# Performance work log

Hardware: AMD Instinct MI355X
Metric: run time of the kernel (lower is better)

Reference implementation:

```python
import jax, jax.numpy as jnp
import numpy as np

N_NODES = 50000
N_EDGES = 800000
D_IN = 256
DIM_H = 256
N_GRAPHS = 500
N_OUT = 10
BN_EPS = 1e-5


def _mlp(h, W1, b1, gamma, beta, mean, var, W2, b2):
    # Linear -> BatchNorm1d (eval, running stats) -> ReLU -> Linear -> ReLU
    h = h @ W1 + b1
    h = (h - mean) * (gamma / jnp.sqrt(var + BN_EPS)) + beta
    h = jax.nn.relu(h)
    return jax.nn.relu(h @ W2 + b2)


def _gin_conv(x, src, dst, params):
    # PyG GINConv with eps=0: out = nn(x + sum_{j in N(i)} x_j)
    agg = jax.ops.segment_sum(x[src], dst, num_segments=N_NODES)
    return _mlp(x + agg, *params)


def setup_inputs() -> dict:
    key = jax.random.key(0)
    ks = jax.random.split(key, 24)
    x = jax.random.normal(ks[0], (N_NODES, D_IN), dtype=jnp.float32)
    edge_index = jax.random.randint(ks[1], (2, N_EDGES), 0, N_NODES, dtype=jnp.int64)
    batch = jnp.sort(jax.random.randint(ks[2], (N_NODES,), 0, N_GRAPHS, dtype=jnp.int64))

    def lin(k, fan_in, fan_out):
        s = 1.0 / np.sqrt(fan_in)
        kw, kb = jax.random.split(k)
        W = jax.random.uniform(kw, (fan_in, fan_out), minval=-s, maxval=s, dtype=jnp.float32)
        b = jax.random.uniform(kb, (fan_out,), minval=-s, maxval=s, dtype=jnp.float32)
        return W, b

    def bn(k, d):
        k1, k2, k3, k4 = jax.random.split(k, 4)
        gamma = 1.0 + 0.1 * jax.random.normal(k1, (d,), dtype=jnp.float32)
        beta = 0.1 * jax.random.normal(k2, (d,), dtype=jnp.float32)
        mean = 0.1 * jax.random.normal(k3, (d,), dtype=jnp.float32)
        var = jax.random.uniform(k4, (d,), minval=0.5, maxval=1.5, dtype=jnp.float32)
        return gamma, beta, mean, var

    W1a, b1a = lin(ks[3], D_IN, DIM_H)
    g1a, be1a, m1a, v1a = bn(ks[4], DIM_H)
    W2a, b2a = lin(ks[5], DIM_H, DIM_H)
    W1b, b1b = lin(ks[6], DIM_H, DIM_H)
    g1b, be1b, m1b, v1b = bn(ks[7], DIM_H)
    W2b, b2b = lin(ks[8], DIM_H, DIM_H)
    lin1_W, lin1_b = lin(ks[9], DIM_H * 2, DIM_H * 3)
    lin2_W, lin2_b = lin(ks[10], DIM_H * 3, N_OUT)

    return dict(x=x, edge_index=edge_index, batch=batch,
                W1a=W1a, b1a=b1a, g1a=g1a, be1a=be1a, m1a=m1a, v1a=v1a, W2a=W2a, b2a=b2a,
                W1b=W1b, b1b=b1b, g1b=g1b, be1b=be1b, m1b=m1b, v1b=v1b, W2b=W2b, b2b=b2b,
                lin1_W=lin1_W, lin1_b=lin1_b, lin2_W=lin2_W, lin2_b=lin2_b)


def reference(x, edge_index, batch,
              W1a, b1a, g1a, be1a, m1a, v1a, W2a, b2a,
              W1b, b1b, g1b, be1b, m1b, v1b, W2b, b2b,
              lin1_W, lin1_b, lin2_W, lin2_b):
    src, dst = edge_index[0], edge_index[1]
    h1 = _gin_conv(x, src, dst, (W1a, b1a, g1a, be1a, m1a, v1a, W2a, b2a))
    h2 = _gin_conv(h1, src, dst, (W1b, b1b, g1b, be1b, m1b, v1b, W2b, b2b))
    p1 = jax.ops.segment_sum(h1, batch, num_segments=N_GRAPHS)  # global_add_pool
    p2 = jax.ops.segment_sum(h2, batch, num_segments=N_GRAPHS)
    h = jnp.concatenate([p1, p2], axis=1)
    h = jax.nn.relu(h @ lin1_W + lin1_b)
    # dropout p=0.6 is identity in eval mode
    h = h @ lin2_W + lin2_b
    return jax.nn.log_softmax(h, axis=1)
```

## Files before the change

### kernel.cpp

```cpp
#include <hip/hip_runtime.h>

#define N_NODES 50000
#define MPAD 50176
#define N_EDGES 800000
#define DIM 256
#define N_GRAPHS 500
#define GPAD 512
#define N_OUT 10
#define BN_EPS 1e-5f
#define SCAN_BS 1024
#define SORT_CAP 96

typedef unsigned int u32;
typedef short bf16x8 __attribute__((ext_vector_type(8)));
typedef unsigned short us8 __attribute__((ext_vector_type(8)));
typedef float f32x4 __attribute__((ext_vector_type(4)));

typedef __attribute__((address_space(1))) const unsigned int gas_u32;
typedef __attribute__((address_space(3))) unsigned int las_u32;

__device__ inline void g2l16(const void* g, void* l) {
    __builtin_amdgcn_global_load_lds((gas_u32*)g, (las_u32*)l, 16, 0, 0);
}

__device__ inline float b2f(unsigned short u) {
    union { u32 i; float f; } c; c.i = ((u32)u) << 16; return c.f;
}
__device__ inline unsigned short f2b(float f) {
    u32 x = __builtin_bit_cast(u32, f);
    return (unsigned short)((x + 0x7FFFu + ((x >> 16) & 1u)) >> 16);
}

__device__ inline int mid_addr(int row, int col) {
    return row * 512 + ((((col >> 3) ^ (row & 31)) << 4) | ((col & 7) << 1));
}

__global__ void prep_misc(int* __restrict__ deg, const int* __restrict__ batch,
                          int* __restrict__ gstart) {
    int bid = blockIdx.x;
    if (bid < 196) {
        int i = bid * 256 + threadIdx.x;
        if (i < N_NODES) deg[i] = 0;
    } else {
        int g = (bid - 196) * 256 + threadIdx.x;
        if (g > N_GRAPHS) return;
        if (g == N_GRAPHS) { gstart[g] = N_NODES; return; }
        int lo = 0, hi = N_NODES;
        while (lo < hi) { int mid = (lo + hi) >> 1; if (batch[mid] < g) lo = mid + 1; else hi = mid; }
        gstart[g] = lo;
    }
}

__global__ void hist_dst(const int* __restrict__ dst, int* __restrict__ deg) {
    int e = blockIdx.x * blockDim.x + threadIdx.x;
    if (e < N_EDGES) atomicAdd(&deg[dst[e]], 1);
}
__global__ void scan_phase1(const int* __restrict__ deg, int* __restrict__ rowptr,
                            int* __restrict__ bsum, int n) {
    __shared__ int sh[SCAN_BS];
    int i = blockIdx.x * SCAN_BS + threadIdx.x;
    int v = (i < n) ? deg[i] : 0;
    sh[threadIdx.x] = v;
    __syncthreads();
    for (int off = 1; off < SCAN_BS; off <<= 1) {
        int t = (threadIdx.x >= off) ? sh[threadIdx.x - off] : 0;
        __syncthreads();
        sh[threadIdx.x] += t;
        __syncthreads();
    }
    if (i < n) rowptr[i] = sh[threadIdx.x] - v;
    if (threadIdx.x == SCAN_BS - 1) bsum[blockIdx.x] = sh[threadIdx.x];
}
__global__ void scan_phase2(int* __restrict__ bsum, int nb) {
    if (threadIdx.x == 0 && blockIdx.x == 0) {
        int run = 0;
        for (int b = 0; b < nb; b++) { int v = bsum[b]; bsum[b] = run; run += v; }
    }
}
__global__ void scan_phase3(int* __restrict__ rowptr, int* __restrict__ cursor,
                            const int* __restrict__ bsum, int n) {
    int i = blockIdx.x * SCAN_BS + threadIdx.x;
    if (i < n) {
        int v = rowptr[i] + bsum[blockIdx.x];
        rowptr[i] = v;
        cursor[i] = v;
    }
    if (i == 0) rowptr[n] = N_EDGES;
}
__global__ void fill_csr(const int* __restrict__ src, const int* __restrict__ dst,
                         int* __restrict__ cursor, unsigned short* __restrict__ col) {
    int e = blockIdx.x * blockDim.x + threadIdx.x;
    if (e < N_EDGES) {
        int p = atomicAdd(&cursor[dst[e]], 1);
        col[p] = (unsigned short)src[e];
    }
}
__global__ void sort_csr(const int* __restrict__ rowptr, unsigned short* __restrict__ col) {
    __shared__ unsigned short buf[4][SORT_CAP];
    int node = blockIdx.x * 4 + (threadIdx.x >> 6);
    if (node >= N_NODES) return;
    int lane = threadIdx.x & 63;
    int w = threadIdx.x >> 6;
    int s = rowptr[node], e = rowptr[node + 1];
    int L = e - s;
    if (L <= 1 || L > SORT_CAP) return;
    for (int i = lane; i < L; i += 64) buf[w][i] = col[s + i];
    asm volatile("s_waitcnt lgkmcnt(0) vmcnt(0)" ::: "memory");
    for (int pass = 0; pass < L; pass++) {
        int base = 2 * lane + (pass & 1);
        if (base + 1 < L) {
            unsigned short a = buf[w][base], b = buf[w][base + 1];
            if (a > b) { buf[w][base] = b; buf[w][base + 1] = a; }
        }
        asm volatile("s_waitcnt lgkmcnt(0)" ::: "memory");
    }
    for (int i = lane; i < L; i += 64) col[s + i] = buf[w][i];
}

__global__ void conv_x(const float4* __restrict__ in, ushort4* __restrict__ out, int n4) {
    int i = blockIdx.x * blockDim.x + threadIdx.x;
    if (i < n4) {
        float4 v = in[i];
        ushort4 o; o.x = f2b(v.x); o.y = f2b(v.y); o.z = f2b(v.z); o.w = f2b(v.w);
        out[i] = o;
    }
}
__global__ void conv_wss(const float* __restrict__ W0, const float* __restrict__ W1,
                         const float* __restrict__ W2, const float* __restrict__ W3,
                         unsigned short* __restrict__ Wt,
                         const float* __restrict__ b1a, const float* __restrict__ g1a,
                         const float* __restrict__ be1a, const float* __restrict__ m1a,
                         const float* __restrict__ v1a,
                         const float* __restrict__ b1b, const float* __restrict__ g1b,
                         const float* __restrict__ be1b, const float* __restrict__ m1b,
                         const float* __restrict__ v1b,
                         float* __restrict__ ss) {
    int mat = blockIdx.y;
    int n = blockIdx.x;
    int k = threadIdx.x;
    if (mat < 4) {
        const float* W = (mat == 0) ? W0 : (mat == 1) ? W1 : (mat == 2) ? W2 : W3;
        Wt[((size_t)mat << 16) + (size_t)n * 256 + k] = f2b(W[(size_t)k * 256 + n]);
    } else if (n == 0) {
        float s = g1a[k] * rsqrtf(v1a[k] + BN_EPS);
        ss[k] = s;
        ss[256 + k] = (b1a[k] - m1a[k]) * s + be1a[k];
    } else if (n == 1) {
        float s = g1b[k] * rsqrtf(v1b[k] + BN_EPS);
        ss[512 + k] = s;
        ss[768 + k] = (b1b[k] - m1b[k]) * s + be1b[k];
    }
}
__global__ void conv_w1h(const float* __restrict__ W, unsigned short* __restrict__ Wh) {
    int n = blockIdx.x;
    int k = threadIdx.x;
    Wh[(size_t)n * 512 + k]       = f2b(W[(size_t)k * 768 + n]);
    Wh[(size_t)n * 512 + 256 + k] = f2b(W[(size_t)(256 + k) * 768 + n]);
}

__global__ void gather_bf(const unsigned short* __restrict__ feat,
                          const unsigned short* __restrict__ col,
                          const int* __restrict__ rowptr,
                          unsigned short* __restrict__ out) {
    int node = blockIdx.x * 4 + (threadIdx.x >> 6);
    if (node >= N_NODES) return;
    int lane = threadIdx.x & 63;
    int half = lane >> 5;
    int d8 = (lane & 31) * 8;
    float acc[8];
    #pragma unroll
    for (int j = 0; j < 8; j++) acc[j] = 0.f;
    if (half == 0) {
        us8 own = *reinterpret_cast<const us8*>(&feat[(size_t)node * DIM + d8]);
        #pragma unroll
        for (int j = 0; j < 8; j++) acc[j] = b2f((unsigned short)own[j]);
    }
    int s = rowptr[node], e = rowptr[node + 1];
    int i = s + half;
    for (; i + 6 < e; i += 8) {
        int n0 = col[i], n1 = col[i + 2], n2 = col[i + 4], n3 = col[i + 6];
        us8 v0 = *reinterpret_cast<const us8*>(&feat[(size_t)n0 * DIM + d8]);
        us8 v1 = *reinterpret_cast<const us8*>(&feat[(size_t)n1 * DIM + d8]);
        us8 v2 = *reinterpret_cast<const us8*>(&feat[(size_t)n2 * DIM + d8]);
        us8 v3 = *reinterpret_cast<const us8*>(&feat[(size_t)n3 * DIM + d8]);
        #pragma unroll
        for (int j = 0; j < 8; j++)
            acc[j] += (b2f((unsigned short)v0[j]) + b2f((unsigned short)v1[j]))
                    + (b2f((unsigned short)v2[j]) + b2f((unsigned short)v3[j]));
    }
    for (; i < e; i += 2) {
        int n0 = col[i];
        us8 v0 = *reinterpret_cast<const us8*>(&feat[(size_t)n0 * DIM + d8]);
        #pragma unroll
        for (int j = 0; j < 8; j++) acc[j] += b2f((unsigned short)v0[j]);
    }
    #pragma unroll
    for (int j = 0; j < 8; j++) acc[j] += __shfl_xor(acc[j], 32, 64);
    if (half == 0) {
        us8 o;
        #pragma unroll
        for (int j = 0; j < 8; j++) o[j] = (short)f2b(acc[j]);
        *reinterpret_cast<us8*>(&out[(size_t)node * DIM + d8]) = o;
    }
}

__global__ __launch_bounds__(256, 2)
void fused_mlp(const unsigned short* __restrict__ A,
               const unsigned short* __restrict__ W1t,
               const unsigned short* __restrict__ W2t,
               const float* __restrict__ scale1,
               const float* __restrict__ shift1,
               const float* __restrict__ shift2,
               unsigned short* __restrict__ H, int M) {
    __shared__ __align__(16) unsigned short Asb[64 * 64];
    __shared__ __align__(16) unsigned short Bsb[256 * 64];
    __shared__ __align__(16) unsigned short midb[64 * 256];

    int t = threadIdx.x;
    int wave = t >> 6, lane = t & 63;
    int m0 = blockIdx.x * 64;
    int wc = wave * 64;
    int rsel = lane & 15;
    int kgrp = lane >> 4;
    int cr = lane >> 4;

    float s1[4], sh1[4], sh2[4];
    #pragma unroll
    for (int n = 0; n < 4; n++) {
        int colg = wc + n * 16 + rsel;
        s1[n]  = scale1[colg];
        sh1[n] = shift1[colg];
        sh2[n] = shift2[colg];
    }

    f32x4 acc[4][4];
    #pragma unroll
    for (int m = 0; m < 4; m++)
        #pragma unroll
        for (int n = 0; n < 4; n++)
            acc[m][n] = (f32x4){0.f, 0.f, 0.f, 0.f};

    int arow0 = t >> 3, achk0 = t & 7;
    int arow1 = (256 + t) >> 3, achk1 = t & 7;
    const char* Abase = (const char*)A + (size_t)m0 * 512;

    for (int ks = 0; ks < 4; ks++) {
        size_t ko = (size_t)ks * 128;
        g2l16(Abase + (size_t)arow0 * 512 + ko + ((achk0 ^ (arow0 & 7)) << 4),
              (char*)Asb + (size_t)t * 16);
        g2l16(Abase + (size_t)arow1 * 512 + ko + ((achk1 ^ (arow1 & 7)) << 4),
              (char*)Asb + (size_t)(256 + t) * 16);
        #pragma unroll
        for (int i = 0; i < 8; i++) {
            int s = i * 256 + t;
            int brow = s >> 3, bchk = s & 7;
            g2l16((const char*)W1t + (size_t)brow * 512 + ko + ((bchk ^ (brow & 7)) << 4),
                  (char*)Bsb + (size_t)s * 16);
        }
        __syncthreads();

        #pragma unroll
        for (int ksub = 0; ksub < 2; ksub++) {
            bf16x8 af[4], bfr[4];
            int kchunk = ksub * 4 + kgrp;
            #pragma unroll
            for (int m = 0; m < 4; m++) {
                int row = m * 16 + rsel;
                af[m] = *(const bf16x8*)((const char*)Asb + (size_t)row * 128
                                         + ((kchunk ^ (row & 7)) << 4));
            }
            #pragma unroll
            for (int n = 0; n < 4; n++) {
                int row = wc + n * 16 + rsel;
                bfr[n] = *(const bf16x8*)((const char*)Bsb + (size_t)row * 128
                                          + ((kchunk ^ (row & 7)) << 4));
            }
            #pragma unroll
            for (int m = 0; m < 4; m++)
                #pragma unroll
                for (int n = 0; n < 4; n++)
                    acc[m][n] = __builtin_amdgcn_mfma_f32_16x16x32_bf16(af[m], bfr[n], acc[m][n], 0, 0, 0);
        }
        __syncthreads();
    }

    #pragma unroll
    for (int n = 0; n < 4; n++) {
        int colg = wc + n * 16 + rsel;
        #pragma unroll
        for (int m = 0; m < 4; m++) {
            int rowb = m * 16 + cr * 4;
            #pragma unroll
            for (int r = 0; r < 4; r++) {
                float v = fmaxf(acc[m][n][r] * s1[n] + sh1[n], 0.f);
                *(unsigned short*)((char*)midb + mid_addr(rowb + r, colg)) = f2b(v);
                acc[m][n][r] = 0.f;
            }
        }
    }

    for (int ks = 0; ks < 4; ks++) {
        size_t ko = (size_t)ks * 128;
        #pragma unroll
        for (int i = 0; i < 8; i++) {
            int s = i * 256 + t;
            int brow = s >> 3, bchk = s & 7;
            g2l16((const char*)W2t + (size_t)brow * 512 + ko + ((bchk ^ (brow & 7)) << 4),
                  (char*)Bsb + (size_t)s * 16);
        }
        __syncthreads();

        #pragma unroll
        for (int ksub = 0; ksub < 2; ksub++) {
            bf16x8 af[4], bfr[4];
            int kchunk = ksub * 4 + kgrp;
            int kcol = ks * 64 + ksub * 32 + kgrp * 8;
            #pragma unroll
            for (int m = 0; m < 4; m++)
                af[m] = *(const bf16x8*)((const char*)midb + mid_addr(m * 16 + rsel, kcol));
            #pragma unroll
            for (int n = 0; n < 4; n++) {
                int row = wc + n * 16 + rsel;
                bfr[n] = *(const bf16x8*)((const char*)Bsb + (size_t)row * 128
                                          + ((kchunk ^ (row & 7)) << 4));
            }
            #pragma unroll
            for (int m = 0; m < 4; m++)
                #pragma unroll
                for (int n = 0; n < 4; n++)
                    acc[m][n] = __builtin_amdgcn_mfma_f32_16x16x32_bf16(af[m], bfr[n], acc[m][n], 0, 0, 0);
        }
        __syncthreads();
    }

    #pragma unroll
    for (int n = 0; n < 4; n++) {
        int colg = wc + n * 16 + rsel;
        #pragma unroll
        for (int m = 0; m < 4; m++) {
            int rowb = m0 + m * 16 + cr * 4;
            #pragma unroll
            for (int r = 0; r < 4; r++) {
                int row = rowb + r;
                if (row < M) {
                    float v = fmaxf(acc[m][n][r] + sh2[n], 0.f);
                    H[(size_t)row * 256 + colg] = f2b(v);
                }
            }
        }
    }
}

__global__ void pool_seg(const unsigned short* __restrict__ h1,
                         const unsigned short* __restrict__ h2,
                         const int* __restrict__ gstart,
                         unsigned short* __restrict__ pcat) {
    __shared__ float red1[8][256];
    __shared__ float red2[8][256];
    int g = blockIdx.x;
    int t = threadIdx.x;
    int sub = t >> 5;
    int d8 = (t & 31) * 8;
    float a1[8], a2[8];
    #pragma unroll
    for (int j = 0; j < 8; j++) { a1[j] = 0.f; a2[j] = 0.f; }
    int s = gstart[g], e = gstart[g + 1];
    for (int n = s + sub; n < e; n += 8) {
        us8 v1 = *reinterpret_cast<const us8*>(&h1[(size_t)n * DIM + d8]);
        us8 v2 = *reinterpret_cast<const us8*>(&h2[(size_t)n * DIM + d8]);
        #pragma unroll
        for (int j = 0; j < 8; j++) {
            a1[j] += b2f((unsigned short)v1[j]);
            a2[j] += b2f((unsigned short)v2[j]);
        }
    }
    #pragma unroll
    for (int j = 0; j < 8; j++) {
        red1[sub][d8 + j] = a1[j];
        red2[sub][d8 + j] = a2[j];
    }
    __syncthreads();
    float o1 = 0.f, o2 = 0.f;
    #pragma unroll
    for (int k = 0; k < 8; k++) { o1 += red1[k][t]; o2 += red2[k][t]; }
    pcat[(size_t)g * 512 + t]       = f2b(o1);
    pcat[(size_t)g * 512 + 256 + t] = f2b(o2);
}

__global__ __launch_bounds__(256)
void head1_mfma(const unsigned short* __restrict__ A,
                const unsigned short* __restrict__ Wh,
                const float* __restrict__ b1,
                float* __restrict__ Hf) {
    __shared__ __align__(16) unsigned short Asb[64 * 64];
    __shared__ __align__(16) unsigned short Bsb[256 * 64];

    int t = threadIdx.x;
    int wave = t >> 6, lane = t & 63;
    int n0 = blockIdx.x * 256;
    int m0 = blockIdx.y * 64;
    int wc = wave * 64;
    int rsel = lane & 15;
    int kgrp = lane >> 4;
    int cr = lane >> 4;

    float bb[4];
    #pragma unroll
    for (int n = 0; n < 4; n++) bb[n] = b1[n0 + wc + n * 16 + rsel];

    f32x4 acc[4][4];
    #pragma unroll
    for (int m = 0; m < 4; m++)
        #pragma unroll
        for (int n = 0; n < 4; n++)
            acc[m][n] = (f32x4){0.f, 0.f, 0.f, 0.f};

    int arow0 = t >> 3, achk0 = t & 7;
    int arow1 = (256 + t) >> 3, achk1 = t & 7;
    const char* Abase = (const char*)A + (size_t)m0 * 1024;

    for (int ks = 0; ks < 8; ks++) {
        size_t ko = (size_t)ks * 128;
        g2l16(Abase + (size_t)arow0 * 1024 + ko + ((achk0 ^ (arow0 & 7)) << 4),
              (char*)Asb + (size_t)t * 16);
        g2l16(Abase + (size_t)arow1 * 1024 + ko + ((achk1 ^ (arow1 & 7)) << 4),
              (char*)Asb + (size_t)(256 + t) * 16);
        #pragma unroll
        for (int i = 0; i < 8; i++) {
            int s = i * 256 + t;
            int brow = s >> 3, bchk = s & 7;
            g2l16((const char*)Wh + (size_t)(n0 + brow) * 1024 + ko + ((bchk ^ (brow & 7)) << 4),
                  (char*)Bsb + (size_t)s * 16);
        }
        __syncthreads();

        #pragma unroll
        for (int ksub = 0; ksub < 2; ksub++) {
            bf16x8 af[4], bfr[4];
            int kchunk = ksub * 4 + kgrp;
            #pragma unroll
            for (int m = 0; m < 4; m++) {
                int row = m * 16 + rsel;
                af[m] = *(const bf16x8*)((const char*)Asb + (size_t)row * 128
                                         + ((kchunk ^ (row & 7)) << 4));
            }
            #pragma unroll
            for (int n = 0; n < 4; n++) {
                int row = wc + n * 16 + rsel;
                bfr[n] = *(const bf16x8*)((const char*)Bsb + (size_t)row * 128
                                          + ((kchunk ^ (row & 7)) << 4));
            }
            #pragma unroll
            for (int m = 0; m < 4; m++)
                #pragma unroll
                for (int n = 0; n < 4; n++)
                    acc[m][n] = __builtin_amdgcn_mfma_f32_16x16x32_bf16(af[m], bfr[n], acc[m][n], 0, 0, 0);
        }
        __syncthreads();
    }

    #pragma unroll
    for (int n = 0; n < 4; n++) {
        int colg = n0 + wc + n * 16 + rsel;
        #pragma unroll
        for (int m = 0; m < 4; m++) {
            int rowb = m0 + m * 16 + cr * 4;
            #pragma unroll
            for (int r = 0; r < 4; r++) {
                int row = rowb + r;
                if (row < N_GRAPHS)
                    Hf[(size_t)row * 768 + colg] = fmaxf(acc[m][n][r] + bb[n], 0.f);
            }
        }
    }
}

__global__ void head2(const float* __restrict__ Hf, const float* __restrict__ W2,
                      const float* __restrict__ b2, float* __restrict__ out) {
    int g = blockIdx.x;
    int lane = threadIdx.x;
    float part[N_OUT];
    #pragma unroll
    for (int o = 0; o < N_OUT; o++) part[o] = 0.f;
    for (int k = lane; k < 768; k += 64) {
        float hv = Hf[(size_t)g * 768 + k];
        #pragma unroll
        for (int o = 0; o < N_OUT; o++) part[o] += hv * W2[(size_t)k * N_OUT + o];
    }
    #pragma unroll
    for (int o = 0; o < N_OUT; o++) {
        #pragma unroll
        for (int off = 32; off > 0; off >>= 1)
            part[o] += __shfl_down(part[o], off, 64);
    }
    if (lane == 0) {
        float logits[N_OUT];
        float mx = -1e30f;
        #pragma unroll
        for (int o = 0; o < N_OUT; o++) { logits[o] = part[o] + b2[o]; mx = fmaxf(mx, logits[o]); }
        float ssum = 0.f;
        #pragma unroll
        for (int o = 0; o < N_OUT; o++) ssum += expf(logits[o] - mx);
        float lse = logf(ssum);
        #pragma unroll
        for (int o = 0; o < N_OUT; o++)
            out[(size_t)g * N_OUT + o] = logits[o] - mx - lse;
    }
}

extern "C" void kernel_launch(void* const* d_in, const int* in_sizes, int n_in,
                              void* d_out, int out_size, void* d_ws, size_t ws_size,
                              hipStream_t stream) {
    const float* x     = (const float*)d_in[0];
    const int*   ei    = (const int*)d_in[1];
    const int*   batch = (const int*)d_in[2];
    const float* W1a = (const float*)d_in[3];
    const float* b1a = (const float*)d_in[4];
    const float* g1a = (const float*)d_in[5];
    const float* be1a= (const float*)d_in[6];
    const float* m1a = (const float*)d_in[7];
    const float* v1a = (const float*)d_in[8];
    const float* W2a = (const float*)d_in[9];
    const float* b2a = (const float*)d_in[10];
    const float* W1b = (const float*)d_in[11];
    const float* b1b = (const float*)d_in[12];
    const float* g1b = (const float*)d_in[13];
    const float* be1b= (const float*)d_in[14];
    const float* m1b = (const float*)d_in[15];
    const float* v1b = (const float*)d_in[16];
    const float* W2b = (const float*)d_in[17];
    const float* b2b = (const float*)d_in[18];
    const float* lin1_W = (const float*)d_in[19];
    const float* lin1_b = (const float*)d_in[20];
    const float* lin2_W = (const float*)d_in[21];
    const float* lin2_b = (const float*)d_in[22];

    const size_t NBUF = (size_t)MPAD * DIM;
    char* ws = (char*)d_ws;
    unsigned short* agg  = (unsigned short*)ws;            ws += NBUF * 2;
    unsigned short* h1   = (unsigned short*)ws;            ws += NBUF * 2;
    unsigned short* h2   = (unsigned short*)ws;            ws += NBUF * 2;
    unsigned short* x_bf = (unsigned short*)ws;            ws += (size_t)N_NODES * DIM * 2;
    unsigned short* Wt   = (unsigned short*)ws;            ws += 4 * 65536 * 2;
    unsigned short* W1h  = (unsigned short*)ws;            ws += (size_t)768 * 512 * 2;
    float* ss    = (float*)ws;                             ws += 4 * 256 * 4;
    unsigned short* pcat = (unsigned short*)ws;            ws += (size_t)GPAD * 512 * 2;
    float* Hf    = (float*)ws;                             ws += (size_t)GPAD * 768 * 4;
    int* deg     = (int*)ws;                               ws += (size_t)N_NODES * 4;
    int* cursor  = (int*)ws;                               ws += (size_t)N_NODES * 4;
    int* rowptr  = (int*)ws;                               ws += (size_t)(N_NODES + 1) * 4;
    int* bsum    = (int*)ws;                               ws += 64 * 4;
    unsigned short* col = (unsigned short*)ws;             ws += (size_t)N_EDGES * 2;
    int* gstart  = (int*)ws;

    const int* srcE = ei;
    const int* dstE = ei + N_EDGES;

    const int nscan = (N_NODES + SCAN_BS - 1) / SCAN_BS;

    prep_misc<<<198, 256, 0, stream>>>(deg, batch, gstart);
    hist_dst<<<(N_EDGES + 255) / 256, 256, 0, stream>>>(dstE, deg);
    scan_phase1<<<nscan, SCAN_BS, 0, stream>>>(deg, rowptr, bsum, N_NODES);
    scan_phase2<<<1, 64, 0, stream>>>(bsum, nscan);
    scan_phase3<<<nscan, SCAN_BS, 0, stream>>>(rowptr, cursor, bsum, N_NODES);
    fill_csr<<<(N_EDGES + 255) / 256, 256, 0, stream>>>(srcE, dstE, cursor, col);
    sort_csr<<<(N_NODES + 3) / 4, 256, 0, stream>>>(rowptr, col);

    conv_x<<<(N_NODES * DIM / 4 + 255) / 256, 256, 0, stream>>>(
        (const float4*)x, (ushort4*)x_bf, N_NODES * DIM / 4);
    dim3 wss_grid(256, 5);
    conv_wss<<<wss_grid, 256, 0, stream>>>(W1a, W2a, W1b, W2b, Wt,
                                           b1a, g1a, be1a, m1a, v1a,
                                           b1b, g1b, be1b, m1b, v1b, ss);
    conv_w1h<<<768, 256, 0, stream>>>(lin1_W, W1h);

    gather_bf<<<(N_NODES + 3) / 4, 256, 0, stream>>>(x_bf, col, rowptr, agg);
    fused_mlp<<<MPAD / 64, 256, 0, stream>>>(agg, Wt + 0 * 65536, Wt + 1 * 65536,
                                             ss, ss + 256, b2a, h1, N_NODES);

    gather_bf<<<(N_NODES + 3) / 4, 256, 0, stream>>>(h1, col, rowptr, agg);
    fused_mlp<<<MPAD / 64, 256, 0, stream>>>(agg, Wt + 2 * 65536, Wt + 3 * 65536,
                                             ss + 512, ss + 768, b2b, h2, N_NODES);

    pool_seg<<<N_GRAPHS, 256, 0, stream>>>(h1, h2, gstart, pcat);
    dim3 h1grid(3, 8);
    head1_mfma<<<h1grid, 256, 0, stream>>>(pcat, W1h, lin1_b, Hf);
    head2<<<N_GRAPHS, 64, 0, stream>>>(Hf, lin2_W, lin2_b, (float*)d_out);
}
```

Measured before the change: 340.2 us.

## Replace per-edge global atomic CSR fill with two-level bucketed scatter

Builds the CSR column array in two passes: edges are first scattered into per-128-node buckets split into 8 partitions, then each bucket is placed by one block using shared-memory cursors. This replaces scattered global atomics on per-node cursors with fewer contended global counters plus LDS atomics, and adds an extra pass through an intermediate buffer. BCAP=512 per slot assumes bounded bucket occupancy, which holds for the random test graph (about 256 edges expected per slot) but could overflow on skewed inputs.

Result: slower. 382.9 us (+12.6%).

```diff
diff --git a/kernel.cpp b/kernel.cpp
--- a/kernel.cpp
+++ b/kernel.cpp
@@ -10,6 +10,9 @@
 #define BN_EPS 1e-5f
 #define SCAN_BS 1024
 #define SORT_CAP 96
+#define NBUCK 391
+#define NPART 8
+#define BCAP 512
 
 typedef unsigned int u32;
 typedef short bf16x8 __attribute__((ext_vector_type(8)));
@@ -36,18 +39,21 @@
 }
 
 __global__ void prep_misc(int* __restrict__ deg, const int* __restrict__ batch,
-                          int* __restrict__ gstart) {
+                          int* __restrict__ gstart, int* __restrict__ bcnt) {
     int bid = blockIdx.x;
     if (bid < 196) {
         int i = bid * 256 + threadIdx.x;
         if (i < N_NODES) deg[i] = 0;
-    } else {
+    } else if (bid < 198) {
         int g = (bid - 196) * 256 + threadIdx.x;
         if (g > N_GRAPHS) return;
         if (g == N_GRAPHS) { gstart[g] = N_NODES; return; }
         int lo = 0, hi = N_NODES;
         while (lo < hi) { int mid = (lo + hi) >> 1; if (batch[mid] < g) lo = mid + 1; else hi = mid; }
         gstart[g] = lo;
+    } else {
+        int i = (bid - 198) * 256 + threadIdx.x;
+        if (i < NBUCK * NPART) bcnt[i] = 0;
     }
 }
 
@@ -77,22 +83,37 @@
         for (int b = 0; b < nb; b++) { int v = bsum[b]; bsum[b] = run; run += v; }
     }
 }
-__global__ void scan_phase3(int* __restrict__ rowptr, int* __restrict__ cursor,
-                            const int* __restrict__ bsum, int n) {
+__global__ void scan_phase3(int* __restrict__ rowptr, const int* __restrict__ bsum, int n) {
     int i = blockIdx.x * SCAN_BS + threadIdx.x;
-    if (i < n) {
-        int v = rowptr[i] + bsum[blockIdx.x];
-        rowptr[i] = v;
-        cursor[i] = v;
-    }
+    if (i < n) rowptr[i] += bsum[blockIdx.x];
     if (i == 0) rowptr[n] = N_EDGES;
 }
-__global__ void fill_csr(const int* __restrict__ src, const int* __restrict__ dst,
-                         int* __restrict__ cursor, unsigned short* __restrict__ col) {
+__global__ void bucket_scatter(const int* __restrict__ src, const int* __restrict__ dst,
+                               int* __restrict__ bcnt, u32* __restrict__ bdata) {
     int e = blockIdx.x * blockDim.x + threadIdx.x;
-    if (e < N_EDGES) {
-        int p = atomicAdd(&cursor[dst[e]], 1);
-        col[p] = (unsigned short)src[e];
+    if (e >= N_EDGES) return;
+    int s = src[e], d = dst[e];
+    int slot = (d >> 7) * NPART + (blockIdx.x & 7);
+    int p = atomicAdd(&bcnt[slot], 1);
+    bdata[(size_t)slot * BCAP + p] = (u32)s | ((u32)(d & 127) << 16);
+}
+__global__ void bucket_fill(const int* __restrict__ rowptr, const int* __restrict__ bcnt,
+                            const u32* __restrict__ bdata, unsigned short* __restrict__ col) {
+    __shared__ int cur[128];
+    int b = blockIdx.x;
+    int node0 = b << 7;
+    int t = threadIdx.x;
+    if (t < 128 && node0 + t < N_NODES) cur[t] = rowptr[node0 + t];
+    __syncthreads();
+    #pragma unroll
+    for (int part = 0; part < NPART; part++) {
+        int slot = b * NPART + part;
+        int cnt = bcnt[slot];
+        for (int j = t; j < cnt; j += 256) {
+            u32 u = bdata[(size_t)slot * BCAP + j];
+            int p = atomicAdd(&cur[u >> 16], 1);
+            col[p] = (unsigned short)(u & 0xFFFFu);
+        }
     }
 }
 __global__ void sort_csr(const int* __restrict__ rowptr, unsigned short* __restrict__ col) {
@@ -547,9 +568,10 @@
     unsigned short* pcat = (unsigned short*)ws;            ws += (size_t)GPAD * 512 * 2;
     float* Hf    = (float*)ws;                             ws += (size_t)GPAD * 768 * 4;
     int* deg     = (int*)ws;                               ws += (size_t)N_NODES * 4;
-    int* cursor  = (int*)ws;                               ws += (size_t)N_NODES * 4;
     int* rowptr  = (int*)ws;                               ws += (size_t)(N_NODES + 1) * 4;
     int* bsum    = (int*)ws;                               ws += 64 * 4;
+    int* bcnt    = (int*)ws;                               ws += (size_t)NBUCK * NPART * 4;
+    u32* bdata   = (u32*)ws;                               ws += (size_t)NBUCK * NPART * BCAP * 4;
     unsigned short* col = (unsigned short*)ws;             ws += (size_t)N_EDGES * 2;
     int* gstart  = (int*)ws;
 
@@ -558,12 +580,13 @@
 
     const int nscan = (N_NODES + SCAN_BS - 1) / SCAN_BS;
 
-    prep_misc<<<198, 256, 0, stream>>>(deg, batch, gstart);
+    prep_misc<<<198 + (NBUCK * NPART + 255) / 256, 256, 0, stream>>>(deg, batch, gstart, bcnt);
     hist_dst<<<(N_EDGES + 255) / 256, 256, 0, stream>>>(dstE, deg);
     scan_phase1<<<nscan, SCAN_BS, 0, stream>>>(deg, rowptr, bsum, N_NODES);
     scan_phase2<<<1, 64, 0, stream>>>(bsum, nscan);
-    scan_phase3<<<nscan, SCAN_BS, 0, stream>>>(rowptr, cursor, bsum, N_NODES);
-    fill_csr<<<(N_EDGES + 255) / 256, 256, 0, stream>>>(srcE, dstE, cursor, col);
+    scan_phase3<<<nscan, SCAN_BS, 0, stream>>>(rowptr, bsum, N_NODES);
+    bucket_scatter<<<(N_EDGES + 255) / 256, 256, 0, stream>>>(srcE, dstE, bcnt, bdata);
+    bucket_fill<<<NBUCK, 256, 0, stream>>>(rowptr, bcnt, bdata, col);
     sort_csr<<<(N_NODES + 3) / 4, 256, 0, stream>>>(rowptr, col);
 
     conv_x<<<(N_NODES * DIM / 4 + 255) / 256, 256, 0, stream>>>(
```
